# Performance work log

Hardware: AMD Instinct MI355X
Metric: run time of the kernel (lower is better)

Reference implementation:

```python
import jax, jax.numpy as jnp
import numpy as np

N, E, F = 25000, 200000, 128


def setup_inputs() -> dict:
    key = jax.random.key(0)
    k1, k2, k3, k4 = jax.random.split(key, 4)
    x = jax.random.normal(k1, (N, F), dtype=jnp.float32)
    edge_index = jax.random.randint(k2, (2, E), 0, N, dtype=jnp.int32)
    batch = jnp.zeros((N,), dtype=jnp.int32)  # single graph
    # EdgePooling.lin = Linear(2F, 1); split weight into src/dst halves
    w_src = jax.random.normal(k3, (F,), dtype=jnp.float32) / np.sqrt(2.0 * F)
    w_dst = jax.random.normal(k4, (F,), dtype=jnp.float32) / np.sqrt(2.0 * F)
    b = jnp.zeros((1,), dtype=jnp.float32)
    return {"x": x, "edge_index": edge_index, "batch": batch,
            "w_src": w_src, "w_dst": w_dst, "b": b}


def reference(x, edge_index, batch, w_src, w_dst, b):
    src, dst = edge_index[0], edge_index[1]
    n = x.shape[0]
    # raw edge score: lin(cat(x[src], x[dst])) == x[src]@w_src + x[dst]@w_dst + b
    raw = x[src] @ w_src + x[dst] @ w_dst + b[0]                 # [E]
    # compute_edge_score_softmax: softmax over edges grouped by dst node
    m = jax.ops.segment_max(raw, dst, num_segments=n)
    z = jnp.exp(raw - m[dst])
    denom = jax.ops.segment_sum(z, dst, num_segments=n)
    e = z / denom[dst] + 0.5                                      # add_to_edge_score=0.5

    # greedy non-overlapping edge contraction, highest score first
    order = jnp.argsort(-e)
    src_s, dst_s, e_s = src[order], dst[order], e[order]

    def step(carry, st):
        matched, cluster, cnt = carry
        s, t = st
        ok = jnp.logical_not(matched[s] | matched[t])
        matched = matched.at[s].set(matched[s] | ok)
        matched = matched.at[t].set(matched[t] | ok)
        cluster = cluster.at[s].set(jnp.where(ok, cnt, cluster[s]))
        cluster = cluster.at[t].set(jnp.where(ok, cnt, cluster[t]))
        out = (ok, jnp.where(ok, cnt, n))  # n = sentinel (dropped later)
        cnt = cnt + ok.astype(cnt.dtype)
        return (matched, cluster, cnt), out

    init = (jnp.zeros((n,), bool), jnp.zeros((n,), jnp.int32), jnp.int32(0))
    (matched, cluster, cnt), (chosen, assigned) = jax.lax.scan(step, init, (src_s, dst_s))

    # leftover (unmatched) nodes become singleton clusters with consecutive ids
    left = jnp.logical_not(matched)
    cluster = jnp.where(left, cnt + jnp.cumsum(left.astype(jnp.int32)) - 1, cluster)
    num_clusters = cnt + left.sum()

    # per-cluster gating score: merged-edge score for pairs, 1.0 for singletons
    cscore = jnp.ones((n,), x.dtype).at[assigned].set(e_s, mode='drop')
    # new node features (padded to n rows; rows >= num_clusters are zero)
    new_x = jax.ops.segment_sum(x, cluster, num_segments=n) * cscore[:, None]
    new_batch = jnp.zeros((n,), batch.dtype).at[cluster].set(batch)
    new_ei = cluster[edge_index]
    new_ei = jnp.where(new_ei[0] == new_ei[1], -1, new_ei)  # mark self-loops invalid
    return new_x, new_ei, new_batch, num_clusters
```

## Files before the change

kernel.cpp:

```cpp
#include <hip/hip_runtime.h>
#include <stdint.h>

typedef unsigned int u32;
typedef unsigned long long u64;
typedef unsigned short u16;
typedef unsigned char u8;

#define FDIM  128
#define NNODE 25000
#define WG    1024
#define RB    64
#define EPT   16
#define RCHUNK (RB*EPT)
#define KBITS 18
#define TAG(r) (((0x3FFFu - (u32)(r)) << KBITS))
#define PRROUNDS 4
#define CB 256
#define CEPT 4
#define CCHUNK (CB*CEPT)
#define HST (256*200)
#define SCCH 1024

__device__ __forceinline__ u32 enc_f32(float f){
  u32 u = __float_as_uint(f);
  return (u & 0x80000000u) ? ~u : (u | 0x80000000u);
}
__device__ __forceinline__ float dec_f32(u32 u){
  u = (u & 0x80000000u) ? (u ^ 0x80000000u) : ~u;
  return __uint_as_float(u);
}

__device__ __forceinline__ float xla_expf(float x){
  x = fminf(x,  88.3762626647950f);
  x = fmaxf(x, -88.3762626647949f);
  float fx = floorf(fmaf(x, 1.44269504088896341f, 0.5f));
  float tmp = __fmul_rn(fx, 0.693359375f);
  float zz  = __fmul_rn(fx, -2.12194440e-4f);
  x = __fsub_rn(x, tmp);
  x = __fsub_rn(x, zz);
  float z2 = __fmul_rn(x, x);
  float y = fmaf(1.9875691500E-4f, x, 1.3981999507E-3f);
  y = fmaf(y, x, 8.3334519073E-3f);
  y = fmaf(y, x, 4.1665795894E-2f);
  y = fmaf(y, x, 1.6666665459E-1f);
  y = fmaf(y, x, 5.0000001201E-1f);
  y = fmaf(y, z2, x);
  y = __fadd_rn(y, 1.0f);
  int n = (int)fx;
  float p2n = __uint_as_float((u32)(n + 127) << 23);
  return __fmul_rn(y, p2n);
}

__global__ __launch_bounds__(256) void k_dots(const float* __restrict__ x,
                      const float* __restrict__ wsrc, const float* __restrict__ wdst,
                      float* __restrict__ ds, float* __restrict__ dd, int N_)
{
  __shared__ float4 w4[64];
  int t = threadIdx.x;
  if (t < 32) w4[t] = ((const float4*)wsrc)[t];
  else if (t < 64) w4[t] = ((const float4*)wdst)[t - 32];
  __syncthreads();
  int v = blockIdx.x * blockDim.x + t;
  if (v >= N_) return;
  const float4* xr = (const float4*)(x + (size_t)v * FDIM);
  float accs = 0.f, accd = 0.f;
  #pragma unroll 4
  for (int k = 0; k < 32; ++k) {
    float4 xv = xr[k], w = w4[k], u = w4[k + 32];
    accs = __fadd_rn(accs, __fmul_rn(xv.x, w.x));
    accs = __fadd_rn(accs, __fmul_rn(xv.y, w.y));
    accs = __fadd_rn(accs, __fmul_rn(xv.z, w.z));
    accs = __fadd_rn(accs, __fmul_rn(xv.w, w.w));
    accd = __fadd_rn(accd, __fmul_rn(xv.x, u.x));
    accd = __fadd_rn(accd, __fmul_rn(xv.y, u.y));
    accd = __fadd_rn(accd, __fmul_rn(xv.z, u.z));
    accd = __fadd_rn(accd, __fmul_rn(xv.w, u.w));
  }
  ds[v] = accs; dd[v] = accd;
}

__global__ __launch_bounds__(RB) void k_rawE(const int* __restrict__ ei, const float* __restrict__ ds,
                       const float* __restrict__ dd, const float* __restrict__ bia,
                       float* __restrict__ raw, u32* __restrict__ m_enc,
                       u64* __restrict__ kvA, u32* __restrict__ hist, int nb, int E_)
{
  __shared__ u32 h[256];
  int t = threadIdx.x, b = blockIdx.x;
  for (int i = t; i < 256; i += RB) h[i] = 0;
  __syncthreads();
  int lo = b * RCHUNK + t * EPT;
  int hi = lo + EPT; if (hi > E_) hi = E_;
  float bv = bia[0];
  for (int e = lo; e < hi; ++e) {
    int s = ei[e], d = ei[E_ + e];
    float r = __fadd_rn(__fadd_rn(ds[s], dd[d]), bv);
    raw[e] = r;
    atomicMax(&m_enc[d], enc_f32(r));
    kvA[e] = ((u64)(u32)d << 32) | (u32)e;
    atomicAdd(&h[(u32)d & 255u], 1u);
  }
  __syncthreads();
  for (int i = t; i < 256; i += RB) hist[(size_t)i * nb + b] = h[i];
}

__global__ __launch_bounds__(RB) void k_rhist(const u64* __restrict__ kv, u32* __restrict__ hist,
                                              int n, int nb, int shift)
{
  __shared__ u32 h[256];
  int t = threadIdx.x, b = blockIdx.x;
  for (int i = t; i < 256; i += RB) h[i] = 0;
  __syncthreads();
  int lo = b * RCHUNK + t * EPT;
  int hi = lo + EPT; if (hi > n) hi = n;
  for (int i = lo; i < hi; ++i) atomicAdd(&h[((u32)(kv[i] >> 32) >> shift) & 255u], 1u);
  __syncthreads();
  for (int i = t; i < 256; i += RB) hist[(size_t)i * nb + b] = h[i];
}

__global__ __launch_bounds__(256) void k_mbs1(const u32* __restrict__ a, u32* __restrict__ bsum, int m)
{
  __shared__ u32 sh[256];
  int t = threadIdx.x, b = blockIdx.x;
  int base = b * SCCH;
  u32 s = 0;
  #pragma unroll
  for (int k = 0; k < SCCH / 256; ++k) { int i = base + t + k * 256; if (i < m) s += a[i]; }
  sh[t] = s; __syncthreads();
  for (int off = 128; off > 0; off >>= 1) { if (t < off) sh[t] += sh[t + off]; __syncthreads(); }
  if (t == 0) bsum[b] = sh[0];
}

__global__ void k_mbs2(u32* __restrict__ bsum, int n)
{
  if (threadIdx.x == 0) {
    u32 run = 0;
    for (int i = 0; i < n; ++i) { u32 v = bsum[i]; bsum[i] = run; run += v; }
  }
}

__global__ __launch_bounds__(256) void k_mbs3(u32* __restrict__ a, const u32* __restrict__ bsum, int m)
{
  __shared__ u32 sh[256];
  const int W = SCCH / 256;
  int t = threadIdx.x, b = blockIdx.x;
  int lo = b * SCCH + t * W;
  u32 v[W];
  u32 c = 0;
  #pragma unroll
  for (int k = 0; k < W; ++k) { int i = lo + k; v[k] = (i < m) ? a[i] : 0u; c += v[k]; }
  u32 mine = c;
  sh[t] = c; __syncthreads();
  for (int off = 1; off < 256; off <<= 1) {
    u32 x = (t >= off) ? sh[t - off] : 0u; __syncthreads();
    sh[t] += x; __syncthreads();
  }
  u32 run = bsum[b] + sh[t] - mine;
  #pragma unroll
  for (int k = 0; k < W; ++k) { int i = lo + k; if (i < m) { a[i] = run; run += v[k]; } }
}

__global__ __launch_bounds__(RB) void k_rscat(const u64* __restrict__ kvin, u64* __restrict__ kvout,
                                              const u32* __restrict__ base, int n, int nb, int shift)
{
  __shared__ u16 h[RB][258];
  __shared__ u32 gbase[256];
  int t = threadIdx.x, b = blockIdx.x;
  for (int i = t; i < RB * 258 / 2; i += RB) ((u32*)h)[i] = 0u;
  __syncthreads();
  int lo = b * RCHUNK + t * EPT;
  int hi = lo + EPT; if (hi > n) hi = n;
  for (int i = lo; i < hi; ++i) { u32 d = ((u32)(kvin[i] >> 32) >> shift) & 255u; h[t][d]++; }
  __syncthreads();
  for (int dg = t; dg < 256; dg += RB) {
    u32 run = 0;
    for (int q = 0; q < RB; ++q) { u16 c = h[q][dg]; h[q][dg] = (u16)run; run += c; }
    gbase[dg] = base[(size_t)dg * nb + b];
  }
  __syncthreads();
  for (int i = lo; i < hi; ++i) {
    u64 kv = kvin[i];
    u32 d = ((u32)(kv >> 32) >> shift) & 255u;
    u32 p = gbase[d] + (u32)h[t][d];
    h[t][d]++;
    kvout[p] = kv;
  }
}

__global__ __launch_bounds__(RB) void k_rscatP(const u64* __restrict__ kvin,
                                               const u32* __restrict__ base, int n, int nb, int shift,
                                               u32* __restrict__ pairByRank, float* __restrict__ scoreByRank,
                                               u8* __restrict__ chosen, u32* __restrict__ nmin)
{
  __shared__ u16 h[RB][258];
  __shared__ u32 gbase[256];
  int t = threadIdx.x, b = blockIdx.x;
  for (int i = t; i < RB * 258 / 2; i += RB) ((u32*)h)[i] = 0u;
  __syncthreads();
  int lo = b * RCHUNK + t * EPT;
  int hi = lo + EPT; if (hi > n) hi = n;
  for (int i = lo; i < hi; ++i) { u32 d = ((u32)(kvin[i] >> 32) >> shift) & 255u; h[t][d]++; }
  __syncthreads();
  for (int dg = t; dg < 256; dg += RB) {
    u32 run = 0;
    for (int q = 0; q < RB; ++q) { u16 c = h[q][dg]; h[q][dg] = (u16)run; run += c; }
    gbase[dg] = base[(size_t)dg * nb + b];
  }
  __syncthreads();
  for (int i = lo; i < hi; ++i) {
    u64 kv = kvin[i];
    u32 key = (u32)(kv >> 32);
    u32 d = (key >> shift) & 255u;
    u32 p = gbase[d] + (u32)h[t][d];
    h[t][d]++;
    u32 sd = (u32)kv;
    pairByRank[p] = sd;
    scoreByRank[p] = dec_f32(~key);
    chosen[p] = 0;
    u32 val = TAG(0) | p;
    atomicMin(&nmin[sd >> 16], val);
    atomicMin(&nmin[sd & 0xFFFFu], val);
  }
}

__global__ void k_scores_seg(const u64* __restrict__ kvS, const float* __restrict__ raw,
                             const u32* __restrict__ m_enc, float* __restrict__ score, int E_)
{
  int i = blockIdx.x * blockDim.x + threadIdx.x;
  if (i >= E_) return;
  u32 d = (u32)(kvS[i] >> 32);
  if (i > 0 && (u32)(kvS[i - 1] >> 32) == d) return;
  float m = dec_f32(m_enc[d]);
  float denom = 0.f;
  int j = i;
  while (j < E_) {
    u64 kv = kvS[j];
    if ((u32)(kv >> 32) != d) break;
    denom = __fadd_rn(denom, xla_expf(__fsub_rn(raw[(u32)kv], m)));
    ++j;
  }
  for (int q = i; q < j; ++q) {
    u32 e = (u32)kvS[q];
    float z = xla_expf(__fsub_rn(raw[e], m));
    score[e] = __fadd_rn(__fdiv_rn(z, denom), 0.5f);
  }
}

__global__ __launch_bounds__(RB) void k_key_score(const float* __restrict__ score, const int* __restrict__ ei,
                            u64* __restrict__ kvB, u32* __restrict__ hist, int nb, int E_)
{
  __shared__ u32 h[256];
  int t = threadIdx.x, b = blockIdx.x;
  for (int i = t; i < 256; i += RB) h[i] = 0;
  __syncthreads();
  int lo = b * RCHUNK + t * EPT;
  int hi = lo + EPT; if (hi > E_) hi = E_;
  for (int e = lo; e < hi; ++e) {
    u32 key = ~enc_f32(score[e]);
    u32 sd = ((u32)ei[e] << 16) | (u32)ei[E_ + e];
    kvB[e] = ((u64)key << 32) | sd;
    atomicAdd(&h[key & 255u], 1u);
  }
  __syncthreads();
  for (int i = t; i < 256; i += RB) hist[(size_t)i * nb + b] = h[i];
}

__global__ void k_choose0(const u32* __restrict__ pairByRank, const u32* __restrict__ nmin,
                          u8* __restrict__ chosen, u8* __restrict__ matched_g, int E_)
{
  int k = blockIdx.x * blockDim.x + threadIdx.x;
  if (k >= E_) return;
  u32 sd = pairByRank[k];
  u32 s = sd >> 16, d = sd & 0xFFFFu;
  u32 myval = TAG(0) | (u32)k;
  if (nmin[s] == myval && nmin[d] == myval) { chosen[k] = 1; matched_g[s] = 1; matched_g[d] = 1; }
}

__global__ void k_compact0(const u32* __restrict__ pairByRank, const u8* __restrict__ matched_g,
                           u64* __restrict__ liveOut, u32* __restrict__ nmin,
                           u32* __restrict__ nlive, int E_)
{
  int k = blockIdx.x * blockDim.x + threadIdx.x;
  int lane = threadIdx.x & 63;
  bool liveE = false; u32 s = 0, d = 0;
  if (k < E_) {
    u32 sd = pairByRank[k];
    s = sd >> 16; d = sd & 0xFFFFu;
    liveE = (!matched_g[s] && !matched_g[d]);
  }
  u64 m = __ballot(liveE);
  if (m != 0ull) {
    int leader = __ffsll((long long)m) - 1;
    u32 base = 0;
    if (lane == leader) base = atomicAdd(nlive, (u32)__popcll(m));
    base = (u32)__shfl((int)base, leader);
    if (liveE) {
      u32 pfx = (u32)__popcll(m & ((1ull << lane) - 1ull));
      liveOut[base + pfx] = ((u64)(u32)k << 32) | ((u64)s << 16) | (u64)d;
      u32 nval = TAG(1) | (u32)k;
      atomicMin(&nmin[s], nval);
      atomicMin(&nmin[d], nval);
    }
  }
}

__global__ void k_chooseR(const u64* __restrict__ liveIn, const u32* __restrict__ nliveIn,
                          const u32* __restrict__ nmin,
                          u8* __restrict__ chosen, u8* __restrict__ matched_g, u32 rtag)
{
  u32 i = blockIdx.x * blockDim.x + threadIdx.x;
  if (i >= *nliveIn) return;
  u64 v = liveIn[i];
  u32 k = (u32)(v >> 32), s = ((u32)v) >> 16, d = (u32)v & 0xFFFFu;
  u32 myval = rtag | k;
  if (nmin[s] == myval && nmin[d] == myval) { chosen[k] = 1; matched_g[s] = 1; matched_g[d] = 1; }
}

__global__ void k_compactR(const u64* __restrict__ liveIn, const u32* __restrict__ nliveIn,
                           const u8* __restrict__ matched_g,
                           u64* __restrict__ liveOut, u32* __restrict__ nmin,
                           u32* __restrict__ nliveOut, u32 ntag)
{
  u32 i = blockIdx.x * blockDim.x + threadIdx.x;
  int lane = threadIdx.x & 63;
  bool liveE = false; u64 v = 0; u32 s = 0, d = 0;
  if (i < *nliveIn) {
    v = liveIn[i];
    s = ((u32)v) >> 16; d = (u32)v & 0xFFFFu;
    liveE = (!matched_g[s] && !matched_g[d]);
  }
  u64 m = __ballot(liveE);
  if (m != 0ull) {
    int leader = __ffsll((long long)m) - 1;
    u32 base = 0;
    if (lane == leader) base = atomicAdd(nliveOut, (u32)__popcll(m));
    base = (u32)__shfl((int)base, leader);
    if (liveE) {
      u32 pfx = (u32)__popcll(m & ((1ull << lane) - 1ull));
      liveOut[base + pfx] = v;
      u32 nval = ntag | (u32)(v >> 32);
      atomicMin(&nmin[s], nval);
      atomicMin(&nmin[d], nval);
    }
  }
}

__global__ __launch_bounds__(WG) void k_match(
    u64* liveA, u64* liveB, const u32* __restrict__ nmin_g, u8* __restrict__ matched_g,
    const u32* __restrict__ nliveIn, u8* __restrict__ chosen, int N_)
{
  __shared__ u32 node_min[NNODE];
  __shared__ u32 s_nlive, s_next;
  const int t = threadIdx.x;
  const int lane = t & 63;

  for (int i = t; i < N_; i += WG) node_min[i] = matched_g[i] ? 0u : nmin_g[i];
  if (t == 0) { s_nlive = *nliveIn; s_next = 0u; }
  __syncthreads();

  u64* LA = liveA; u64* LB = liveB;
  u32 r = PRROUNDS;
  while (true) {
    u32 nl = s_nlive;
    if (nl == 0u || r > 16000u) break;
    const u32 tag  = TAG(r);
    const u32 ntag = TAG(r + 1);

    for (u32 i = (u32)t; i < nl; i += WG) {
      u64 v = LA[i];
      u32 k = (u32)(v >> 32);
      u32 s = ((u32)v) >> 16, d = (u32)v & 0xFFFFu;
      u32 myval = tag | k;
      if (node_min[s] == myval && node_min[d] == myval) {
        chosen[k] = 1; node_min[s] = 0u; node_min[d] = 0u;
      }
    }
    __syncthreads();

    for (u32 i0 = (u32)(t & ~63); i0 < nl; i0 += WG) {
      u32 i = i0 + (u32)lane;
      bool liveE = false; u64 v = 0;
      u32 s = 0, d = 0;
      if (i < nl) {
        v = LA[i];
        s = ((u32)v) >> 16; d = (u32)v & 0xFFFFu;
        liveE = (node_min[s] != 0u && node_min[d] != 0u);
      }
      u64 m = __ballot(liveE);
      if (m != 0ull) {
        int leader = __ffsll((long long)m) - 1;
        u32 baseIdx = 0;
        if (lane == leader) baseIdx = atomicAdd(&s_next, (u32)__popcll(m));
        baseIdx = (u32)__shfl((int)baseIdx, leader);
        if (liveE) {
          u32 pfx = (u32)__popcll(m & ((1ull << lane) - 1ull));
          LB[baseIdx + pfx] = v;
          u32 nval = ntag | (u32)(v >> 32);
          atomicMin(&node_min[s], nval);
          atomicMin(&node_min[d], nval);
        }
      }
    }
    __syncthreads();
    if (t == 0) { s_nlive = s_next; s_next = 0u; }
    { u64* tmp = LA; LA = LB; LB = tmp; }
    ++r;
    __syncthreads();
  }

  for (int i = t; i < N_; i += WG) matched_g[i] = (node_min[i] == 0u) ? 1 : 0;
}

__global__ __launch_bounds__(CB) void k_sums(const u8* __restrict__ chosen, u32* __restrict__ csum, int E_,
                                             const u8* __restrict__ matched, u32* __restrict__ nsum, int N_,
                                             int nbc)
{
  __shared__ u32 sh[CB];
  int t = threadIdx.x, b = blockIdx.x;
  const u8* src; int n; u32* dst; int bb;
  if (b < nbc) { src = chosen; n = E_; dst = csum; bb = b; }
  else         { src = matched; n = N_; dst = nsum; bb = b - nbc; }
  int lo = bb * CCHUNK + t * CEPT;
  int hi = lo + CEPT; if (hi > n) hi = n;
  u32 c = 0;
  if (b < nbc) { for (int i = lo; i < hi; ++i) c += src[i]; }
  else         { for (int i = lo; i < hi; ++i) c += (src[i] ? 0u : 1u); }
  sh[t] = c; __syncthreads();
  for (int off = CB / 2; off > 0; off >>= 1) { if (t < off) sh[t] += sh[t + off]; __syncthreads(); }
  if (t == 0) dst[bb] = sh[0];
}

__global__ void k_scan2(u32* __restrict__ csum, int nbc, u32* __restrict__ nsum, int nbn,
                        u32* __restrict__ cnts)
{
  if (threadIdx.x == 0) {
    u32 run = 0;
    for (int i = 0; i < nbc; ++i) { u32 v = csum[i]; csum[i] = run; run += v; }
    cnts[4] = run;
    u32 run2 = 0;
    for (int i = 0; i < nbn; ++i) { u32 v = nsum[i]; nsum[i] = run2; run2 += v; }
    cnts[3] = run + run2;
  }
}

__global__ __launch_bounds__(CB) void k_assign(const u8* __restrict__ chosen, const u32* __restrict__ csum,
    const u32* __restrict__ pairByRank, const float* __restrict__ scoreByRank, int E_,
    const u8* __restrict__ matched, const u32* __restrict__ nsum, int N_,
    const u32* __restrict__ cnts,
    int* __restrict__ cluster, u32* __restrict__ pairA, u32* __restrict__ pairB,
    float* __restrict__ cscore, int nbc)
{
  __shared__ u32 sh[CB];
  int t = threadIdx.x, b = blockIdx.x;
  if (b < nbc) {
    int lo = b * CCHUNK + t * CEPT;
    int hi = lo + CEPT; if (hi > E_) hi = E_;
    u32 c = 0;
    for (int i = lo; i < hi; ++i) c += chosen[i];
    u32 mine = c;
    sh[t] = c; __syncthreads();
    for (int off = 1; off < CB; off <<= 1) {
      u32 a = (t >= off) ? sh[t - off] : 0u; __syncthreads();
      sh[t] += a; __syncthreads();
    }
    u32 run = csum[b] + sh[t] - mine;
    for (int i = lo; i < hi; ++i) {
      if (chosen[i]) {
        u32 cc = run++;
        u32 sd = pairByRank[i];
        u32 sv = sd >> 16, dv = sd & 0xFFFFu;
        cluster[sv] = (int)cc; cluster[dv] = (int)cc;
        pairA[cc] = sv; pairB[cc] = dv; cscore[cc] = scoreByRank[i];
      }
    }
  } else {
    int bb = b - nbc;
    int lo = bb * CCHUNK + t * CEPT;
    int hi = lo + CEPT; if (hi > N_) hi = N_;
    u32 c = 0;
    for (int i = lo; i < hi; ++i) c += (matched[i] ? 0u : 1u);
    u32 mine = c;
    sh[t] = c; __syncthreads();
    for (int off = 1; off < CB; off <<= 1) {
      u32 a = (t >= off) ? sh[t - off] : 0u; __syncthreads();
      sh[t] += a; __syncthreads();
    }
    u32 run = cnts[4] + nsum[bb] + sh[t] - mine;
    for (int v = lo; v < hi; ++v) {
      if (!matched[v]) {
        u32 cc = run++;
        cluster[v] = (int)cc;
        pairA[cc] = (u32)v; pairB[cc] = (u32)v; cscore[cc] = 1.0f;
      }
    }
  }
}

__global__ void k_newx(const float* __restrict__ x, const u32* __restrict__ pairA,
                       const u32* __restrict__ pairB, const float* __restrict__ cscore,
                       const u32* __restrict__ cnts, float* __restrict__ out, int N_)
{
  int j = blockIdx.x * blockDim.x + threadIdx.x;
  int total = N_ * (FDIM / 4);
  if (j >= total) return;
  u32 c = (u32)(j >> 5);
  int q = (j & 31) * 4;
  float4 o;
  if (c >= cnts[3]) {
    o.x = 0.f; o.y = 0.f; o.z = 0.f; o.w = 0.f;
  } else {
    u32 a = pairA[c], bb = pairB[c];
    float cs = cscore[c];
    const float4 va = *(const float4*)(x + (size_t)a * FDIM + q);
    if (a == bb) {
      o.x = __fmul_rn(va.x, cs); o.y = __fmul_rn(va.y, cs);
      o.z = __fmul_rn(va.z, cs); o.w = __fmul_rn(va.w, cs);
    } else {
      const float4 vb = *(const float4*)(x + (size_t)bb * FDIM + q);
      o.x = __fmul_rn(__fadd_rn(va.x, vb.x), cs);
      o.y = __fmul_rn(__fadd_rn(va.y, vb.y), cs);
      o.z = __fmul_rn(__fadd_rn(va.z, vb.z), cs);
      o.w = __fmul_rn(__fadd_rn(va.w, vb.w), cs);
    }
  }
  *(float4*)(out + (size_t)c * FDIM + q) = o;
}

__global__ void k_newei(const int* __restrict__ ei, const int* __restrict__ cluster,
                        const u32* __restrict__ cnts, float* __restrict__ out, int N_, int E_)
{
  int e = blockIdx.x * blockDim.x + threadIdx.x;
  if (e >= E_) return;
  int c0 = cluster[ei[e]];
  int c1 = cluster[ei[E_ + e]];
  if (c0 == c1) { c0 = -1; c1 = -1; }
  size_t base = (size_t)N_ * FDIM;
  out[base + e] = (float)c0;
  out[base + E_ + e] = (float)c1;
  if (e < N_) out[base + 2 * (size_t)E_ + e] = 0.0f;
  if (e == 0) out[base + 2 * (size_t)E_ + N_] = (float)cnts[3];
}

extern "C" void kernel_launch(void* const* d_in, const int* in_sizes, int n_in,
                              void* d_out, int out_size, void* d_ws, size_t ws_size,
                              hipStream_t stream)
{
  const float* x    = (const float*)d_in[0];
  const int*   ei   = (const int*)d_in[1];
  const float* wsrc = (const float*)d_in[3];
  const float* wdst = (const float*)d_in[4];
  const float* b    = (const float*)d_in[5];
  const int N = in_sizes[0] / FDIM;
  const int E = in_sizes[1] / 2;

  u32* w = (u32*)d_ws;
  float* raw   = (float*)w;      w += E;
  float* score = (float*)w;      w += E;
  u64* kvA = (u64*)w;            w += 2 * E;
  u64* kvB = (u64*)w;            w += 2 * E;
  float* ds = (float*)w;         w += N;
  float* dd = (float*)w;         w += N;
  int* cluster = (int*)w;        w += N;
  u32* pairA = w;                w += N;
  u32* pairB = w;                w += N;
  float* cscore = (float*)w;     w += N;
  u32* nmin = w;                 w += N;
  u32* csum = w;                 w += 256;
  u32* nsum = w;                 w += 64;
  u32* bsum = w;                 w += 256;
  u32* hist = w;                 w += HST;
  u32* zeros = w;
  u32* m_enc  = w;               w += N;
  u8*  matched_g = (u8*)w;       w += (N + 3) / 4;
  u32* cnts = w;                 w += 16;
  size_t zwords = (size_t)(w - zeros);

  u64* liveA = (u64*)d_out;
  u64* liveB = (u64*)((u32*)d_out + 2 * (size_t)E);
  u32* pairByRank  = (u32*)d_out + 4 * (size_t)E;
  float* scoreByRank = (float*)((u32*)d_out + 5 * (size_t)E);
  u8* chosen = (u8*)((u32*)d_out + 6 * (size_t)E);

  const int TB = 256;
  const int gridE = (E + TB - 1) / TB;
  const int gridN = (N + TB - 1) / TB;
  const int nb = (E + RCHUNK - 1) / RCHUNK;
  const int m  = nb * 256;
  const int nsb = (m + SCCH - 1) / SCCH;
  const int nbc = (E + CCHUNK - 1) / CCHUNK;
  const int nbn = (N + CCHUNK - 1) / CCHUNK;

  hipMemsetAsync(zeros, 0, zwords * 4, stream);
  hipMemsetAsync(nmin, 0xFF, (size_t)N * 4, stream);

  #define HSCAN() do { \
    k_mbs1<<<nsb, 256, 0, stream>>>(hist, bsum, m); \
    k_mbs2<<<1, 64, 0, stream>>>(bsum, nsb); \
    k_mbs3<<<nsb, 256, 0, stream>>>(hist, bsum, m); \
  } while (0)

  k_dots<<<gridN, TB, 0, stream>>>(x, wsrc, wdst, ds, dd, N);
  k_rawE<<<nb, RB, 0, stream>>>(ei, ds, dd, b, raw, m_enc, kvA, hist, nb, E);

  HSCAN();
  k_rscat<<<nb, RB, 0, stream>>>(kvA, kvB, hist, E, nb, 0);
  k_rhist<<<nb, RB, 0, stream>>>(kvB, hist, E, nb, 8);
  HSCAN();
  k_rscat<<<nb, RB, 0, stream>>>(kvB, kvA, hist, E, nb, 8);

  k_scores_seg<<<gridE, TB, 0, stream>>>(kvA, raw, m_enc, score, E);

  k_key_score<<<nb, RB, 0, stream>>>(score, ei, kvB, hist, nb, E);
  HSCAN();
  k_rscat<<<nb, RB, 0, stream>>>(kvB, kvA, hist, E, nb, 0);
  k_rhist<<<nb, RB, 0, stream>>>(kvA, hist, E, nb, 8);
  HSCAN();
  k_rscat<<<nb, RB, 0, stream>>>(kvA, kvB, hist, E, nb, 8);
  k_rhist<<<nb, RB, 0, stream>>>(kvB, hist, E, nb, 16);
  HSCAN();
  k_rscatP<<<nb, RB, 0, stream>>>(kvB, hist, E, nb, 16,
                                  pairByRank, scoreByRank, chosen, nmin);

  k_choose0<<<gridE, TB, 0, stream>>>(pairByRank, nmin, chosen, matched_g, E);
  k_compact0<<<gridE, TB, 0, stream>>>(pairByRank, matched_g, liveB, nmin, &cnts[8], E);

  u64* Lin = liveB; u64* Lout = liveA;
  for (int r = 1; r < PRROUNDS; ++r) {
    k_chooseR<<<gridE, TB, 0, stream>>>(Lin, &cnts[8 + r - 1], nmin, chosen, matched_g, TAG(r));
    k_compactR<<<gridE, TB, 0, stream>>>(Lin, &cnts[8 + r - 1], matched_g, Lout, nmin,
                                         &cnts[8 + r], TAG(r + 1));
    u64* tmp = Lin; Lin = Lout; Lout = tmp;
  }

  k_match<<<1, WG, 0, stream>>>(Lin, Lout, nmin, matched_g, &cnts[8 + PRROUNDS - 1],
                                chosen, N);

  k_sums<<<nbc + nbn, CB, 0, stream>>>(chosen, csum, E, matched_g, nsum, N, nbc);
  k_scan2<<<1, 64, 0, stream>>>(csum, nbc, nsum, nbn, cnts);
  k_assign<<<nbc + nbn, CB, 0, stream>>>(chosen, csum, pairByRank, scoreByRank, E,
                                         matched_g, nsum, N, cnts,
                                         cluster, pairA, pairB, cscore, nbc);

  k_newx<<<(N * (FDIM / 4) + TB - 1) / TB, TB, 0, stream>>>(x, pairA, pairB, cscore, cnts, (float*)d_out, N);
  k_newei<<<gridE, TB, 0, stream>>>(ei, cluster, cnts, (float*)d_out, N, E);
}
```

Baseline: 387.8 us.

## Fold single-thread scans into consumer kernels and merge output kernels

Removes the serial one-thread prefix kernels (k_mbs2, k_scan2). Each consumer block now reduces the preceding block sums itself in shared memory to get its offset. Rewrites the round-0 choose step to iterate over nodes instead of edges, and fuses the new_x and new_ei kernels into one launch. This cuts launches and serial tail latency, at the cost of redundant per-block reductions, which assume the block-sum count fits in 256.

Measured after the change: 338.0 us. 12.8% less time.

```diff
diff --git a/kernel.cpp b/kernel.cpp
--- a/kernel.cpp
+++ b/kernel.cpp
@@ -13,6 +13,7 @@
 #define EPT   16
 #define RCHUNK (RB*EPT)
 #define KBITS 18
+#define RMASK ((1u << KBITS) - 1u)
 #define TAG(r) (((0x3FFFu - (u32)(r)) << KBITS))
 #define PRROUNDS 4
 #define CB 256
@@ -130,19 +131,17 @@
   if (t == 0) bsum[b] = sh[0];
 }
 
-__global__ void k_mbs2(u32* __restrict__ bsum, int n)
-{
-  if (threadIdx.x == 0) {
-    u32 run = 0;
-    for (int i = 0; i < n; ++i) { u32 v = bsum[i]; bsum[i] = run; run += v; }
-  }
-}
-
 __global__ __launch_bounds__(256) void k_mbs3(u32* __restrict__ a, const u32* __restrict__ bsum, int m)
 {
   __shared__ u32 sh[256];
+  __shared__ u32 s_off;
   const int W = SCCH / 256;
   int t = threadIdx.x, b = blockIdx.x;
+  sh[t] = (t < b) ? bsum[t] : 0u;
+  __syncthreads();
+  for (int off = 128; off > 0; off >>= 1) { if (t < off) sh[t] += sh[t + off]; __syncthreads(); }
+  if (t == 0) s_off = sh[0];
+  __syncthreads();
   int lo = b * SCCH + t * W;
   u32 v[W];
   u32 c = 0;
@@ -154,7 +153,7 @@
     u32 x = (t >= off) ? sh[t - off] : 0u; __syncthreads();
     sh[t] += x; __syncthreads();
   }
-  u32 run = bsum[b] + sh[t] - mine;
+  u32 run = s_off + sh[t] - mine;
   #pragma unroll
   for (int k = 0; k < W; ++k) { int i = lo + k; if (i < m) { a[i] = run; run += v[k]; } }
 }
@@ -264,15 +263,21 @@
   for (int i = t; i < 256; i += RB) hist[(size_t)i * nb + b] = h[i];
 }
 
-__global__ void k_choose0(const u32* __restrict__ pairByRank, const u32* __restrict__ nmin,
-                          u8* __restrict__ chosen, u8* __restrict__ matched_g, int E_)
-{
-  int k = blockIdx.x * blockDim.x + threadIdx.x;
-  if (k >= E_) return;
+__global__ void k_choose0N(const u32* __restrict__ pairByRank, const u32* __restrict__ nmin,
+                           u8* __restrict__ chosen, u8* __restrict__ matched_g, int N_)
+{
+  int v = blockIdx.x * blockDim.x + threadIdx.x;
+  if (v >= N_) return;
+  u32 mv = nmin[v];
+  if (mv == 0xFFFFFFFFu) return;
+  u32 k = mv & RMASK;
   u32 sd = pairByRank[k];
   u32 s = sd >> 16, d = sd & 0xFFFFu;
-  u32 myval = TAG(0) | (u32)k;
-  if (nmin[s] == myval && nmin[d] == myval) { chosen[k] = 1; matched_g[s] = 1; matched_g[d] = 1; }
+  u32 other = ((u32)v == s) ? d : s;
+  if (nmin[other] == mv) {
+    matched_g[v] = 1;
+    if ((u32)v == s) chosen[k] = 1;
+  }
 }
 
 __global__ void k_compact0(const u32* __restrict__ pairByRank, const u8* __restrict__ matched_g,
@@ -429,29 +434,22 @@
   if (t == 0) dst[bb] = sh[0];
 }
 
-__global__ void k_scan2(u32* __restrict__ csum, int nbc, u32* __restrict__ nsum, int nbn,
-                        u32* __restrict__ cnts)
-{
-  if (threadIdx.x == 0) {
-    u32 run = 0;
-    for (int i = 0; i < nbc; ++i) { u32 v = csum[i]; csum[i] = run; run += v; }
-    cnts[4] = run;
-    u32 run2 = 0;
-    for (int i = 0; i < nbn; ++i) { u32 v = nsum[i]; nsum[i] = run2; run2 += v; }
-    cnts[3] = run + run2;
-  }
-}
-
 __global__ __launch_bounds__(CB) void k_assign(const u8* __restrict__ chosen, const u32* __restrict__ csum,
     const u32* __restrict__ pairByRank, const float* __restrict__ scoreByRank, int E_,
     const u8* __restrict__ matched, const u32* __restrict__ nsum, int N_,
-    const u32* __restrict__ cnts,
+    u32* __restrict__ cnts,
     int* __restrict__ cluster, u32* __restrict__ pairA, u32* __restrict__ pairB,
-    float* __restrict__ cscore, int nbc)
+    float* __restrict__ cscore, int nbc, int nbn)
 {
   __shared__ u32 sh[CB];
+  __shared__ u32 s_off;
   int t = threadIdx.x, b = blockIdx.x;
   if (b < nbc) {
+    sh[t] = (t < b) ? csum[t] : 0u;
+    __syncthreads();
+    for (int off = CB / 2; off > 0; off >>= 1) { if (t < off) sh[t] += sh[t + off]; __syncthreads(); }
+    if (t == 0) s_off = sh[0];
+    __syncthreads();
     int lo = b * CCHUNK + t * CEPT;
     int hi = lo + CEPT; if (hi > E_) hi = E_;
     u32 c = 0;
@@ -462,7 +460,7 @@
       u32 a = (t >= off) ? sh[t - off] : 0u; __syncthreads();
       sh[t] += a; __syncthreads();
     }
-    u32 run = csum[b] + sh[t] - mine;
+    u32 run = s_off + sh[t] - mine;
     for (int i = lo; i < hi; ++i) {
       if (chosen[i]) {
         u32 cc = run++;
@@ -474,6 +472,18 @@
     }
   } else {
     int bb = b - nbc;
+    sh[t] = ((t < nbc) ? csum[t] : 0u) + ((t >= nbc && t < nbc + bb) ? nsum[t - nbc] : 0u);
+    __syncthreads();
+    for (int off = CB / 2; off > 0; off >>= 1) { if (t < off) sh[t] += sh[t + off]; __syncthreads(); }
+    if (t == 0) s_off = sh[0];
+    __syncthreads();
+    if (bb == 0) {
+      sh[t] = ((t < nbc) ? csum[t] : 0u) + ((t >= nbc && t < nbc + nbn) ? nsum[t - nbc] : 0u);
+      __syncthreads();
+      for (int off = CB / 2; off > 0; off >>= 1) { if (t < off) sh[t] += sh[t + off]; __syncthreads(); }
+      if (t == 0) cnts[3] = sh[0];
+      __syncthreads();
+    }
     int lo = bb * CCHUNK + t * CEPT;
     int hi = lo + CEPT; if (hi > N_) hi = N_;
     u32 c = 0;
@@ -484,7 +494,7 @@
       u32 a = (t >= off) ? sh[t - off] : 0u; __syncthreads();
       sh[t] += a; __syncthreads();
     }
-    u32 run = cnts[4] + nsum[bb] + sh[t] - mine;
+    u32 run = s_off + sh[t] - mine;
     for (int v = lo; v < hi; ++v) {
       if (!matched[v]) {
         u32 cc = run++;
@@ -495,49 +505,50 @@
   }
 }
 
-__global__ void k_newx(const float* __restrict__ x, const u32* __restrict__ pairA,
-                       const u32* __restrict__ pairB, const float* __restrict__ cscore,
-                       const u32* __restrict__ cnts, float* __restrict__ out, int N_)
-{
-  int j = blockIdx.x * blockDim.x + threadIdx.x;
-  int total = N_ * (FDIM / 4);
-  if (j >= total) return;
-  u32 c = (u32)(j >> 5);
-  int q = (j & 31) * 4;
-  float4 o;
-  if (c >= cnts[3]) {
-    o.x = 0.f; o.y = 0.f; o.z = 0.f; o.w = 0.f;
+__global__ __launch_bounds__(256) void k_out(const float* __restrict__ x, const u32* __restrict__ pairA,
+                     const u32* __restrict__ pairB, const float* __restrict__ cscore,
+                     const u32* __restrict__ cnts,
+                     const int* __restrict__ ei, const int* __restrict__ cluster,
+                     float* __restrict__ out, int N_, int E_, int nxb)
+{
+  int b = blockIdx.x, t = threadIdx.x;
+  if (b < nxb) {
+    int j = b * 256 + t;
+    int total = N_ * (FDIM / 4);
+    if (j >= total) return;
+    u32 c = (u32)(j >> 5);
+    int q = (j & 31) * 4;
+    float4 o;
+    if (c >= cnts[3]) {
+      o.x = 0.f; o.y = 0.f; o.z = 0.f; o.w = 0.f;
+    } else {
+      u32 a = pairA[c], bb = pairB[c];
+      float cs = cscore[c];
+      const float4 va = *(const float4*)(x + (size_t)a * FDIM + q);
+      if (a == bb) {
+        o.x = __fmul_rn(va.x, cs); o.y = __fmul_rn(va.y, cs);
+        o.z = __fmul_rn(va.z, cs); o.w = __fmul_rn(va.w, cs);
+      } else {
+        const float4 vb = *(const float4*)(x + (size_t)bb * FDIM + q);
+        o.x = __fmul_rn(__fadd_rn(va.x, vb.x), cs);
+        o.y = __fmul_rn(__fadd_rn(va.y, vb.y), cs);
+        o.z = __fmul_rn(__fadd_rn(va.z, vb.z), cs);
+        o.w = __fmul_rn(__fadd_rn(va.w, vb.w), cs);
+      }
+    }
+    *(float4*)(out + (size_t)c * FDIM + q) = o;
   } else {
-    u32 a = pairA[c], bb = pairB[c];
-    float cs = cscore[c];
-    const float4 va = *(const float4*)(x + (size_t)a * FDIM + q);
-    if (a == bb) {
-      o.x = __fmul_rn(va.x, cs); o.y = __fmul_rn(va.y, cs);
-      o.z = __fmul_rn(va.z, cs); o.w = __fmul_rn(va.w, cs);
-    } else {
-      const float4 vb = *(const float4*)(x + (size_t)bb * FDIM + q);
-      o.x = __fmul_rn(__fadd_rn(va.x, vb.x), cs);
-      o.y = __fmul_rn(__fadd_rn(va.y, vb.y), cs);
-      o.z = __fmul_rn(__fadd_rn(va.z, vb.z), cs);
-      o.w = __fmul_rn(__fadd_rn(va.w, vb.w), cs);
-    }
-  }
-  *(float4*)(out + (size_t)c * FDIM + q) = o;
-}
-
-__global__ void k_newei(const int* __restrict__ ei, const int* __restrict__ cluster,
-                        const u32* __restrict__ cnts, float* __restrict__ out, int N_, int E_)
-{
-  int e = blockIdx.x * blockDim.x + threadIdx.x;
-  if (e >= E_) return;
-  int c0 = cluster[ei[e]];
-  int c1 = cluster[ei[E_ + e]];
-  if (c0 == c1) { c0 = -1; c1 = -1; }
-  size_t base = (size_t)N_ * FDIM;
-  out[base + e] = (float)c0;
-  out[base + E_ + e] = (float)c1;
-  if (e < N_) out[base + 2 * (size_t)E_ + e] = 0.0f;
-  if (e == 0) out[base + 2 * (size_t)E_ + N_] = (float)cnts[3];
+    int e = (b - nxb) * 256 + t;
+    if (e >= E_) return;
+    int c0 = cluster[ei[e]];
+    int c1 = cluster[ei[E_ + e]];
+    if (c0 == c1) { c0 = -1; c1 = -1; }
+    size_t base = (size_t)N_ * FDIM;
+    out[base + e] = (float)c0;
+    out[base + E_ + e] = (float)c1;
+    if (e < N_) out[base + 2 * (size_t)E_ + e] = 0.0f;
+    if (e == 0) out[base + 2 * (size_t)E_ + N_] = (float)cnts[3];
+  }
 }
 
 extern "C" void kernel_launch(void* const* d_in, const int* in_sizes, int n_in,
@@ -588,13 +599,13 @@
   const int nsb = (m + SCCH - 1) / SCCH;
   const int nbc = (E + CCHUNK - 1) / CCHUNK;
   const int nbn = (N + CCHUNK - 1) / CCHUNK;
+  const int nxb = (N * (FDIM / 4) + TB - 1) / TB;
 
   hipMemsetAsync(zeros, 0, zwords * 4, stream);
   hipMemsetAsync(nmin, 0xFF, (size_t)N * 4, stream);
 
   #define HSCAN() do { \
     k_mbs1<<<nsb, 256, 0, stream>>>(hist, bsum, m); \
-    k_mbs2<<<1, 64, 0, stream>>>(bsum, nsb); \
     k_mbs3<<<nsb, 256, 0, stream>>>(hist, bsum, m); \
   } while (0)
 
@@ -620,7 +631,7 @@
   k_rscatP<<<nb, RB, 0, stream>>>(kvB, hist, E, nb, 16,
                                   pairByRank, scoreByRank, chosen, nmin);
 
-  k_choose0<<<gridE, TB, 0, stream>>>(pairByRank, nmin, chosen, matched_g, E);
+  k_choose0N<<<gridN, TB, 0, stream>>>(pairByRank, nmin, chosen, matched_g, N);
   k_compact0<<<gridE, TB, 0, stream>>>(pairByRank, matched_g, liveB, nmin, &cnts[8], E);
 
   u64* Lin = liveB; u64* Lout = liveA;
@@ -635,11 +646,10 @@
                                 chosen, N);
 
   k_sums<<<nbc + nbn, CB, 0, stream>>>(chosen, csum, E, matched_g, nsum, N, nbc);
-  k_scan2<<<1, 64, 0, stream>>>(csum, nbc, nsum, nbn, cnts);
   k_assign<<<nbc + nbn, CB, 0, stream>>>(chosen, csum, pairByRank, scoreByRank, E,
                                          matched_g, nsum, N, cnts,
-                                         cluster, pairA, pairB, cscore, nbc);
-
-  k_newx<<<(N * (FDIM / 4) + TB - 1) / TB, TB, 0, stream>>>(x, pairA, pairB, cscore, cnts, (float*)d_out, N);
-  k_newei<<<gridE, TB, 0, stream>>>(ei, cluster, cnts, (float*)d_out, N, E);
-}
+                                         cluster, pairA, pairB, cscore, nbc, nbn);
+
+  k_out<<<nxb + gridE, TB, 0, stream>>>(x, pairA, pairB, cscore, cnts, ei, cluster,
+                                        (float*)d_out, N, E, nxb);
+}
```
